# Performance work log

Measured on AMD Instinct MI355X. Metric: run time of the kernel, lower is better.

## Reference

```python
import jax, jax.numpy as jnp
import numpy as np

K = 10
EPS = 1e-5
SLOPE = 0.01
B, FIN, FOUT, N = 16, 128, 128, 2048


def _bn(x, g, b, axes):
    # training-mode batchnorm over given axes (channel dim is axis 1)
    m = jnp.mean(x, axis=axes, keepdims=True)
    v = jnp.var(x, axis=axes, keepdims=True)
    sh = [1] * x.ndim
    sh[1] = -1
    return (x - m) * jax.lax.rsqrt(v + EPS) * g.reshape(sh) + b.reshape(sh)


def _lrelu(x):
    return jnp.where(x >= 0, x, SLOPE * x)


def _conv1x1(x, W, b):
    return jnp.einsum('bcnk,oc->bonk', x, W) + b[None, :, None, None]


def _forward(x, pc, Wf, bf, gf, betaf, Wx, bx, gx, betax, Wa1, ba1, ga1, beta_a1, Wa2, ba2, ga2, beta_a2, Wi, bi, gi, beta_i, W2, b2, g2, beta2):
    Bsz, Fin, Npts = x.shape
    k = K
    # --- kNN graph build: pairwise sq-dist via bmm, full sort, drop self ---
    sq = jnp.sum(x * x, axis=1)  # [B,N]
    dist = -2.0 * jnp.einsum('bdn,bdm->bnm', x, x) + sq[:, :, None] + sq[:, None, :]
    idx = jnp.argsort(dist, axis=2)[:, :, 1:k + 1]  # [B,N,k]
    gather = jax.vmap(lambda f, i: f[:, i])  # [C,N],[N,k] -> [C,N,k]
    nbr = gather(x, idx)
    nbr_xyz = gather(pc, idx)
    e_fea = jnp.concatenate([jnp.broadcast_to(x[..., None], (Bsz, Fin, Npts, k)), nbr - x[..., None]], axis=1)   # [B,2Fin,N,k]
    e_xyz = jnp.concatenate([jnp.broadcast_to(pc[..., None], (Bsz, 3, Npts, k)), nbr_xyz - pc[..., None]], axis=1)  # [B,6,N,k]
    # --- bilateral attention weights ---
    w = _lrelu(_bn(_conv1x1(e_fea, Wf, bf), gf, betaf, (0, 2, 3))) * _lrelu(_bn(_conv1x1(e_xyz, Wx, bx), gx, betax, (0, 2, 3)))
    w = _lrelu(_bn(_conv1x1(w, Wa1, ba1), ga1, beta_a1, (0, 2, 3)))
    w = _lrelu(_bn(_conv1x1(w, Wa2, ba2), ga2, beta_a2, (0, 2, 3)))
    w = jax.nn.softmax(w, axis=-1)  # [B,2Fin,N,k]
    # --- interpolation conv over neighbour axis (kernel [1, k//2+1]) ---
    inte = jax.lax.conv_general_dilated(e_fea, Wi, (1, 1), 'VALID', dimension_numbers=('NCHW', 'OIHW', 'NCHW')) + bi[None, :, None, None]
    inte = _lrelu(_bn(inte, gi, beta_i, (0, 2, 3)))  # [B,4Fin,N,k-k//2]
    inte = jnp.transpose(inte, (0, 2, 1, 3)).reshape(Bsz, Npts, 2 * Fin, k)  # channel-pair interleave, same layout as torch .view
    inte = jnp.transpose(inte, (0, 2, 1, 3)) * w  # [B,2Fin,N,k]
    merge = jnp.concatenate([e_fea, inte], axis=3)  # [B,2Fin,N,2k]
    # conv2: kernel [1,2k] spans full width -> width-1 output, as einsum
    out = jnp.einsum('bcnw,ocw->bon', merge, W2[:, :, 0, :]) + b2[None, :, None]  # [B,2Fout,N]
    out = jnp.maximum(_bn(out, g2, beta2, (0, 2)), 0.0)
    Fout = out.shape[1] // 2
    return out.reshape(Bsz, Fout, 2 * Npts)


def setup_inputs() -> dict:
    ks = jax.random.split(jax.random.key(0), 10)
    s = 0.05
    return {
        'x': jax.random.normal(ks[0], (B, FIN, N), jnp.float32),
        'pc': jax.random.normal(ks[1], (B, 3, N), jnp.float32),
        'Wf': jax.random.normal(ks[2], (16, 2 * FIN), jnp.float32) * s,
        'bf': jnp.zeros((16,), jnp.float32), 'gf': jnp.ones((16,), jnp.float32), 'betaf': jnp.zeros((16,), jnp.float32),
        'Wx': jax.random.normal(ks[3], (16, 6), jnp.float32) * s,
        'bx': jnp.zeros((16,), jnp.float32), 'gx': jnp.ones((16,), jnp.float32), 'betax': jnp.zeros((16,), jnp.float32),
        'Wa1': jax.random.normal(ks[4], (64, 16), jnp.float32) * s,
        'ba1': jnp.zeros((64,), jnp.float32), 'ga1': jnp.ones((64,), jnp.float32), 'beta_a1': jnp.zeros((64,), jnp.float32),
        'Wa2': jax.random.normal(ks[5], (2 * FIN, 64), jnp.float32) * s,
        'ba2': jnp.zeros((2 * FIN,), jnp.float32), 'ga2': jnp.ones((2 * FIN,), jnp.float32), 'beta_a2': jnp.zeros((2 * FIN,), jnp.float32),
        'Wi': jax.random.normal(ks[6], (4 * FIN, 2 * FIN, 1, K // 2 + 1), jnp.float32) * s,
        'bi': jnp.zeros((4 * FIN,), jnp.float32), 'gi': jnp.ones((4 * FIN,), jnp.float32), 'beta_i': jnp.zeros((4 * FIN,), jnp.float32),
        'W2': jax.random.normal(ks[7], (2 * FOUT, 2 * FIN, 1, 2 * K), jnp.float32) * s,
        'b2': jnp.zeros((2 * FOUT,), jnp.float32), 'g2': jnp.ones((2 * FOUT,), jnp.float32), 'beta2': jnp.zeros((2 * FOUT,), jnp.float32),
    }


def reference(x, pc, Wf, bf, gf, betaf, Wx, bx, gx, betax, Wa1, ba1, ga1, beta_a1, Wa2, ba2, ga2, beta_a2, Wi, bi, gi, beta_i, W2, b2, g2, beta2):
    return _forward(x, pc, Wf, bf, gf, betaf, Wx, bx, gx, betax, Wa1, ba1, ga1, beta_a1, Wa2, ba2, ga2, beta_a2, Wi, bi, gi, beta_i, W2, b2, g2, beta2)
```

## Files before the change

kernel.cpp:

```cpp
#include <hip/hip_runtime.h>
#include <hip/hip_bf16.h>
#include <cstdio>
#include <cstddef>

#define B_    16
#define FIN_  128
#define N_    2048
#define K_    10
#define EPS_  1e-5f
#define SLOPE_ 0.01f

typedef float f32x4 __attribute__((ext_vector_type(4)));
typedef short s16x8 __attribute__((ext_vector_type(8)));
typedef short s16x4 __attribute__((ext_vector_type(4)));

constexpr int SUM_F=0,   SS_F=16,   SUM_X=32,  SS_X=48;
constexpr int SUM_A1=64, SS_A1=128, SUM_A2=192,SS_A2=448;
constexpr int SUM_I=704, SS_I=1216, SUM_O=1728,SS_O=1984;
constexpr int SCALE_F=2240, SHIFT_F=2256, SCALE_X=2272, SHIFT_X=2288;
constexpr int SCALE_A1=2304, SHIFT_A1=2368, SCALE_A2=2432, SHIFT_A2=2688;
constexpr int SCALE_I=2944, SHIFT_I=3456, SCALE_O=3968, SHIFT_O=4224;
constexpr int STATS_TOTAL=4480;

constexpr int KW2_ = 3968;
constexpr int CHUNK_ = 8192;

__device__ __forceinline__ float lrelu(float v){ return v >= 0.f ? v : SLOPE_*v; }
__device__ __forceinline__ float wave_sum(float v){
  #pragma unroll
  for (int o = 32; o > 0; o >>= 1) v += __shfl_down(v, o, 64);
  return v;
}
__device__ __forceinline__ unsigned short f2bf(float f){
  __hip_bfloat16 h = __float2bfloat16(f);
  return *reinterpret_cast<unsigned short*>(&h);
}
__device__ __forceinline__ float bf2f(unsigned short u){
  __hip_bfloat16 h = *reinterpret_cast<__hip_bfloat16*>(&u);
  return __bfloat162float(h);
}

__global__ void k_zero(float* s){
  for (int i = threadIdx.x; i < STATS_TOTAL; i += 256) s[i] = 0.f;
}

__global__ __launch_bounds__(256) void k_xt(const float* __restrict__ x, float* __restrict__ xT){
  __shared__ float t[32][33];
  const int b = blockIdx.z;
  const int c0 = blockIdx.x*32, n0 = blockIdx.y*32;
  const int tx = threadIdx.x & 31, ty = threadIdx.x >> 5;
  #pragma unroll
  for (int s = 0; s < 32; s += 8)
    t[ty+s][tx] = x[((size_t)b*FIN_ + c0+ty+s)*N_ + n0 + tx];
  __syncthreads();
  #pragma unroll
  for (int s = 0; s < 32; s += 8)
    xT[((size_t)b*N_ + n0+ty+s)*FIN_ + c0 + tx] = t[tx][ty+s];
}

__global__ __launch_bounds__(256) void k_sq(const float* __restrict__ x, float* __restrict__ sq){
  int id = blockIdx.x*256 + threadIdx.x;
  int b = id >> 11, n = id & (N_-1);
  const float* xb = x + (size_t)b*FIN_*N_ + n;
  float part[16];
  #pragma unroll
  for (int p = 0; p < 16; ++p){
    float a = 0.f;
    #pragma unroll
    for (int q = 0; q < 8; ++q){
      float v = xb[(size_t)(p + 16*q)*N_];
      a = __fmaf_rn(v, v, a);
    }
    part[p] = a;
  }
  #pragma unroll
  for (int off = 8; off > 0; off >>= 1){
    #pragma unroll
    for (int l = 0; l < off; ++l)
      part[l] = __fadd_rn(part[l], part[l+off]);
  }
  sq[id] = part[0];
}

__global__ __launch_bounds__(256, 2) void k_knn(const float* __restrict__ x, const float* __restrict__ sq,
                                                int* __restrict__ idx){
  __shared__ __align__(16) char smem[61440];
  float* xi = (float*)smem;
  const int b = blockIdx.y, i0 = blockIdx.x*64;
  const float* xb = x + (size_t)b*FIN_*N_;
  for (int t = threadIdx.x; t < FIN_*64; t += 256){
    int c = t >> 6, ii = t & 63;
    xi[t] = xb[(size_t)c*N_ + i0 + ii];
  }
  __syncthreads();
  const int ty = threadIdx.x >> 4;
  const int tx = threadIdx.x & 15;
  const int ibase = ty*4;
  const f32x4 sqi = *(const f32x4*)&sq[b*N_ + i0 + ibase];
  float bd[4][10]; int bi[4][10];
  #pragma unroll
  for (int ii=0;ii<4;++ii)
    #pragma unroll
    for (int s=0;s<10;++s){ bd[ii][s]=1e30f; bi[ii][s]=-1; }

  for (int j0 = 0; j0 < N_; j0 += 64){
    const int jb = j0 + tx*4;
    const float* xjp = xb + jb;
    f32x4 acc[4] = {};
    #pragma unroll 8
    for (int c = 0; c < FIN_; ++c){
      const f32x4 a  = *(const f32x4*)&xi[c*64 + ibase];
      const f32x4 bb = *(const f32x4*)&xjp[(size_t)c*N_];
      #pragma unroll
      for (int ii=0;ii<4;++ii){
        #pragma unroll
        for (int m=0;m<4;++m)
          acc[ii][m] = __fmaf_rn(a[ii], bb[m], acc[ii][m]);
      }
    }
    const f32x4 sqj = *(const f32x4*)&sq[b*N_ + jb];
    #pragma unroll
    for (int ii=0;ii<4;++ii){
      const int i = i0 + ibase + ii;
      #pragma unroll
      for (int m=0;m<4;++m){
        int j = jb + m;
        float d = __fadd_rn(__fadd_rn(__fmul_rn(-2.f, acc[ii][m]), sqi[ii]), sqj[m]);
        if (j == i) d = 1e30f;
        if (d < bd[ii][9]){
          bd[ii][9] = d; bi[ii][9] = j;
          #pragma unroll
          for (int s = 9; s > 0; --s){
            if (bd[ii][s] < bd[ii][s-1]){
              float td = bd[ii][s]; bd[ii][s] = bd[ii][s-1]; bd[ii][s-1] = td;
              int ti = bi[ii][s]; bi[ii][s] = bi[ii][s-1]; bi[ii][s-1] = ti;
            }
          }
        }
      }
    }
  }

  __syncthreads();
  float* dbuf = (float*)smem;
  unsigned short* ibuf = (unsigned short*)(smem + 40960);
  #pragma unroll
  for (int ii=0;ii<4;++ii)
    #pragma unroll
    for (int s=0;s<10;++s){
      dbuf[(tx*10+s)*64 + ibase+ii] = bd[ii][s];
      ibuf[(tx*10+s)*64 + ibase+ii] = (unsigned short)bi[ii][s];
    }
  __syncthreads();
  if (threadIdx.x < 64){
    const int rr = threadIdx.x;
    int p[16];
    #pragma unroll
    for (int qq=0;qq<16;++qq) p[qq]=0;
    int* op = idx + ((size_t)b*N_ + i0 + rr)*K_;
    for (int s = 0; s < K_; ++s){
      float dm = 1e38f; int im = 0x7fffffff; int qm = 0;
      #pragma unroll
      for (int qq = 0; qq < 16; ++qq){
        int pq = p[qq];
        float d  = (pq < 10) ? dbuf[(qq*10+pq)*64 + rr] : 1e38f;
        int   jd = (pq < 10) ? (int)ibuf[(qq*10+pq)*64 + rr] : 0x7fffffff;
        bool take = (d < dm) || (d == dm && jd < im);
        if (take){ dm = d; im = jd; qm = qq; }
      }
      #pragma unroll
      for (int qq = 0; qq < 16; ++qq) if (qm == qq) p[qq]++;
      op[s] = im;
    }
  }
}

__global__ __launch_bounds__(256) void k_fx_stats(const float* __restrict__ xT, const float* __restrict__ pc,
                                                  const int* __restrict__ idx,
                                                  const float* __restrict__ Wf, const float* __restrict__ Wx,
                                                  float* __restrict__ stats, float* __restrict__ ytmp){
  __shared__ float wfT[256*16];
  __shared__ float wxT[6*16];
  for (int t = threadIdx.x; t < 256*16; t += 256){ int c = t >> 4, o = t & 15; wfT[t] = Wf[o*256 + c]; }
  if (threadIdx.x < 96){ int cc = threadIdx.x >> 4, o = threadIdx.x & 15; wxT[cc*16+o] = Wx[o*6+cc]; }
  __syncthreads();
  const int id = blockIdx.x*256 + threadIdx.x;
  const int b = id >> 11, n = id & (N_-1);
  const float* xs = xT + (size_t)id*FIN_;
  const float* pb = pc + (size_t)b*3*N_;
  float yc[16];
  #pragma unroll
  for (int o=0;o<16;++o) yc[o]=0.f;
  for (int c=0;c<FIN_;c+=4){
    const f32x4 v4 = *(const f32x4*)&xs[c];
    #pragma unroll
    for (int e=0;e<4;++e){
      float v = v4[e];
      #pragma unroll
      for (int o=0;o<16;++o) yc[o] += wfT[(c+e)*16+o]*v;
    }
  }
  float p0=pb[n], p1=pb[N_+n], p2=pb[2*N_+n];
  float sf[16], ssf[16], sx[16], ssx[16];
  #pragma unroll
  for (int o=0;o<16;++o){ sf[o]=0.f;ssf[o]=0.f;sx[o]=0.f;ssx[o]=0.f; }
  for (int kk=0;kk<K_;++kk){
    int j = idx[(size_t)id*K_ + kk];
    const float* xj = xT + ((size_t)b*N_ + j)*FIN_;
    float y[16];
    #pragma unroll
    for (int o=0;o<16;++o) y[o]=yc[o];
    for (int c=0;c<FIN_;c+=4){
      const f32x4 a4 = *(const f32x4*)&xj[c];
      const f32x4 s4 = *(const f32x4*)&xs[c];
      #pragma unroll
      for (int e=0;e<4;++e){
        float d = a4[e]-s4[e];
        #pragma unroll
        for (int o=0;o<16;++o) y[o] += wfT[(128+c+e)*16+o]*d;
      }
    }
    float q0=pb[j]-p0, q1=pb[N_+j]-p1, q2=pb[2*N_+j]-p2;
    float vx[16];
    #pragma unroll
    for (int o=0;o<16;++o){
      vx[o] = wxT[0*16+o]*p0 + wxT[1*16+o]*p1 + wxT[2*16+o]*p2
            + wxT[3*16+o]*q0 + wxT[4*16+o]*q1 + wxT[5*16+o]*q2;
    }
    #pragma unroll
    for (int o=0;o<16;++o){
      sf[o]+=y[o]; ssf[o]+=y[o]*y[o];
      sx[o]+=vx[o]; ssx[o]+=vx[o]*vx[o];
    }
    float* yt = ytmp + ((size_t)id*K_ + kk)*32;
    #pragma unroll
    for (int o=0;o<16;++o){ yt[o] = y[o]; yt[16+o] = vx[o]; }
  }
  #pragma unroll
  for (int o=0;o<16;++o){
    float v;
    v = wave_sum(sf[o]);  if ((threadIdx.x&63)==0) atomicAdd(&stats[SUM_F+o], v);
    v = wave_sum(ssf[o]); if ((threadIdx.x&63)==0) atomicAdd(&stats[SS_F+o], v);
    v = wave_sum(sx[o]);  if ((threadIdx.x&63)==0) atomicAdd(&stats[SUM_X+o], v);
    v = wave_sum(ssx[o]); if ((threadIdx.x&63)==0) atomicAdd(&stats[SS_X+o], v);
  }
}

__global__ void k_finalize(float* stats, int sumoff, int ssoff, int nch, float cnt_inv,
                           const float* __restrict__ g, const float* __restrict__ bt,
                           int scoff, int shoff){
  int c = threadIdx.x;
  if (c < nch){
    float mean = stats[sumoff+c]*cnt_inv;
    float var  = stats[ssoff+c]*cnt_inv - mean*mean;
    float rstd = rsqrtf(var + EPS_);
    float sc = g[c]*rstd;
    stats[scoff+c] = sc;
    stats[shoff+c] = bt[c] - mean*sc;
  }
}

__global__ __launch_bounds__(256) void k_wapply(const float* __restrict__ ytmp, const float* __restrict__ stats,
                                                float* __restrict__ wprod){
  __shared__ float s4[64];
  if (threadIdx.x < 64) s4[threadIdx.x] = stats[SCALE_F + threadIdx.x];
  __syncthreads();
  const int e = blockIdx.x*256 + threadIdx.x;
  const float* yt = ytmp + (size_t)e*32;
  float* wp = wprod + (size_t)e*16;
  #pragma unroll
  for (int o=0;o<16;++o){
    float a  = lrelu(yt[o]*s4[o] + s4[16+o]);
    float bb = lrelu(yt[16+o]*s4[32+o] + s4[48+o]);
    wp[o] = a*bb;
  }
}

__global__ __launch_bounds__(256) void k_a1_stats(const float* __restrict__ wprod, const float* __restrict__ Wa1,
                                                  float* __restrict__ stats){
  __shared__ float wp[64*16];
  const int oc = threadIdx.x & 63, sub = threadIdx.x >> 6;
  float wa[16];
  #pragma unroll
  for (int j = 0; j < 16; ++j) wa[j] = Wa1[oc*16+j];
  float s = 0.f, ss = 0.f;
  for (int tile = blockIdx.x; tile < 5120; tile += gridDim.x){
    __syncthreads();
    for (int t = threadIdx.x; t < 1024; t += 256) wp[t] = wprod[(size_t)tile*1024 + t];
    __syncthreads();
    for (int p = sub*16; p < sub*16+16; ++p){
      float y = 0.f;
      #pragma unroll
      for (int j = 0; j < 16; ++j) y += wa[j]*wp[p*16+j];
      s += y; ss += y*y;
    }
  }
  atomicAdd(&stats[SUM_A1+oc], s);
  atomicAdd(&stats[SS_A1+oc], ss);
}

__global__ __launch_bounds__(256) void k_a2_stats(const float* __restrict__ wprod, const float* __restrict__ Wa1,
                                                  const float* __restrict__ Wa2, float* __restrict__ stats){
  __shared__ float wp[64*16];
  __shared__ float a1t[64*64];
  __shared__ float wa1T[16*64];
  __shared__ float sc1[64], sh1[64];
  for (int t=threadIdx.x;t<1024;t+=256){ int j=t&63, jj=t>>6; wa1T[jj*64+j] = Wa1[j*16+jj]; }
  if (threadIdx.x < 64){ sc1[threadIdx.x]=stats[SCALE_A1+threadIdx.x]; sh1[threadIdx.x]=stats[SHIFT_A1+threadIdx.x]; }
  const int oc = threadIdx.x;
  float wa2[64];
  #pragma unroll
  for (int j=0;j<64;++j) wa2[j] = Wa2[oc*64+j];
  float s=0.f, ss=0.f;
  for (int tile = blockIdx.x; tile < 5120; tile += gridDim.x){
    __syncthreads();
    for (int t=threadIdx.x;t<1024;t+=256) wp[t] = wprod[(size_t)tile*1024 + t];
    __syncthreads();
    for (int t=threadIdx.x;t<4096;t+=256){
      int p = t >> 6, j = t & 63;
      float yv=0.f;
      #pragma unroll
      for (int jj=0;jj<16;++jj) yv += wa1T[jj*64+j]*wp[p*16+jj];
      a1t[t] = lrelu(yv*sc1[j]+sh1[j]);
    }
    __syncthreads();
    #pragma unroll 4
    for (int p=0;p<64;++p){
      float yv=0.f;
      #pragma unroll
      for (int j=0;j<64;++j) yv += wa2[j]*a1t[p*64+j];
      s += yv; ss += yv*yv;
    }
  }
  atomicAdd(&stats[SUM_A2+oc], s);
  atomicAdd(&stats[SS_A2+oc], ss);
}

__global__ __launch_bounds__(256) void k_prepAi(const float* __restrict__ Wi, unsigned short* __restrict__ Ai){
  const int total = 512*896;
  for (int e = blockIdx.x*256 + threadIdx.x; e < total; e += gridDim.x*256){
    int o = e / 896, k = e - o*896;
    float v;
    if (k < 768){
      int u = k >> 7, c = k & 127;
      v = Wi[(size_t)o*1536 + (128+c)*6 + u];
    } else {
      const float* p = &Wi[(size_t)o*1536 + (size_t)(k-768)*6];
      v = p[0]+p[1]+p[2]+p[3]+p[4]+p[5];
    }
    Ai[e] = f2bf(v);
  }
}

__global__ __launch_bounds__(256) void k_prepA2(const float* __restrict__ W2,
                                                unsigned short* __restrict__ A2hi,
                                                unsigned short* __restrict__ A2lo){
  const int total = 256*KW2_;
  for (int e = blockIdx.x*256 + threadIdx.x; e < total; e += gridDim.x*256){
    int oc = e / KW2_, k = e - oc*KW2_;
    const float* wr = &W2[(size_t)oc*5120];
    float v;
    if (k < 2560){
      int o = k & 511, t5 = k >> 9;
      int cch = o >> 1, w = (o & 1)*5 + t5;
      v = wr[cch*20 + 10 + w];
    } else if (k < 3840){
      int kk = k - 2560; int w = kk >> 7, c = kk & 127;
      v = wr[(128+c)*20 + w];
    } else {
      int c = k - 3840;
      float s = 0.f;
      #pragma unroll
      for (int w = 0; w < 10; ++w) s += wr[c*20+w] - wr[(128+c)*20+w];
      v = s;
    }
    unsigned short hi = f2bf(v);
    float lo = v - bf2f(hi);
    A2hi[e] = hi;
    A2lo[e] = f2bf(lo);
  }
}

__global__ __launch_bounds__(256) void k_gather(const float* __restrict__ xT, const int* __restrict__ idx,
                                                unsigned short* __restrict__ Bd, int pxbase){
  const int e = blockIdx.x*256 + threadIdx.x;
  const int pxl = e >> 4, sub = e & 15;
  const int px = pxbase + pxl;
  const int c0 = sub*8;
  const float* xs = xT + (size_t)px*FIN_ + c0;
  const f32x4 s0 = *(const f32x4*)&xs[0];
  const f32x4 s1 = *(const f32x4*)&xs[4];
  unsigned short* bo = Bd + (size_t)pxl*1408;
  const size_t bb = (size_t)(px >> 11)*N_*FIN_;
  const int* ip = idx + (size_t)px*K_;
  #pragma unroll
  for (int w = 0; w < 10; ++w){
    int j = ip[w];
    const float* xj = xT + bb + (size_t)j*FIN_ + c0;
    const f32x4 a0 = *(const f32x4*)&xj[0];
    const f32x4 a1 = *(const f32x4*)&xj[4];
    unsigned short tw[8];
    tw[0]=f2bf(a0.x-s0.x); tw[1]=f2bf(a0.y-s0.y); tw[2]=f2bf(a0.z-s0.z); tw[3]=f2bf(a0.w-s0.w);
    tw[4]=f2bf(a1.x-s1.x); tw[5]=f2bf(a1.y-s1.y); tw[6]=f2bf(a1.z-s1.z); tw[7]=f2bf(a1.w-s1.w);
    *(s16x8*)&bo[w*128 + c0] = *(const s16x8*)tw;
  }
  unsigned short tw[8];
  tw[0]=f2bf(s0.x); tw[1]=f2bf(s0.y); tw[2]=f2bf(s0.z); tw[3]=f2bf(s0.w);
  tw[4]=f2bf(s1.x); tw[5]=f2bf(s1.y); tw[6]=f2bf(s1.z); tw[7]=f2bf(s1.w);
  *(s16x8*)&bo[1280 + c0] = *(const s16x8*)tw;
}

__global__ __launch_bounds__(256) void k_gemmI(const unsigned short* __restrict__ Bd,
                                               const unsigned short* __restrict__ Ai,
                                               __hip_bfloat16* __restrict__ ybuf, float* __restrict__ stats,
                                               int pxbase){
  __shared__ __align__(16) unsigned short As[128*72];
  __shared__ __align__(16) unsigned short Bs[128*72];
  const int o0 = blockIdx.x * 128;
  const int c0 = blockIdx.y * 128;
  const int t5 = blockIdx.z;
  const int rowA = threadIdx.x >> 1;
  const int kA   = (threadIdx.x & 1)*32;
  const unsigned short* arow = Ai + (size_t)(o0+rowA)*896 + kA;
  const int colJ = threadIdx.x >> 1;
  const int kB   = (threadIdx.x & 1)*32;
  const unsigned short* brow = Bd + (size_t)(c0 + colJ)*1408;
  const int wave = threadIdx.x >> 6, lane = threadIdx.x & 63;
  const int quad = lane >> 4, l16 = lane & 15;
  const int wm = wave & 1, wn = wave >> 1;

  f32x4 acc[4][4] = {};

  for (int k0 = 0; k0 < 896; k0 += 64){
    __syncthreads();
    {
      unsigned short* dst = &As[rowA*72 + kA];
      *(s16x8*)&dst[0]  = *(const s16x8*)&arow[k0+0];
      *(s16x8*)&dst[8]  = *(const s16x8*)&arow[k0+8];
      *(s16x8*)&dst[16] = *(const s16x8*)&arow[k0+16];
      *(s16x8*)&dst[24] = *(const s16x8*)&arow[k0+24];
    }
    {
      const int kk = k0 + kB;
      const unsigned short* src = brow + ((kk < 768) ? ((t5 + (kk >> 7))*128 + (kk & 127))
                                                     : (1280 + (kk - 768)));
      unsigned short* dst = &Bs[colJ*72 + kB];
      *(s16x8*)&dst[0]  = *(const s16x8*)&src[0];
      *(s16x8*)&dst[8]  = *(const s16x8*)&src[8];
      *(s16x8*)&dst[16] = *(const s16x8*)&src[16];
      *(s16x8*)&dst[24] = *(const s16x8*)&src[24];
    }
    __syncthreads();
    #pragma unroll
    for (int ks = 0; ks < 2; ++ks){
      s16x8 af[4], bfr[4];
      #pragma unroll
      for (int mt = 0; mt < 4; ++mt)
        af[mt] = *(const s16x8*)&As[(wm*64 + mt*16 + l16)*72 + ks*32 + quad*8];
      #pragma unroll
      for (int nt = 0; nt < 4; ++nt)
        bfr[nt] = *(const s16x8*)&Bs[(wn*64 + nt*16 + l16)*72 + ks*32 + quad*8];
      #pragma unroll
      for (int mt = 0; mt < 4; ++mt)
        #pragma unroll
        for (int nt = 0; nt < 4; ++nt)
          acc[mt][nt] = __builtin_amdgcn_mfma_f32_16x16x32_bf16(af[mt], bfr[nt], acc[mt][nt], 0, 0, 0);
    }
  }

  __syncthreads();
  float* red = (float*)As;
  red[threadIdx.x] = 0.f;
  __syncthreads();
  #pragma unroll
  for (int mt = 0; mt < 4; ++mt){
    const int rowLbase = wm*64 + mt*16 + quad*4;
    #pragma unroll
    for (int reg = 0; reg < 4; ++reg){
      float s = 0.f, ss = 0.f;
      #pragma unroll
      for (int nt = 0; nt < 4; ++nt){ float v = acc[mt][nt][reg]; s += v; ss += v*v; }
      atomicAdd(&red[(rowLbase+reg)*2+0], s);
      atomicAdd(&red[(rowLbase+reg)*2+1], ss);
    }
  }
  #pragma unroll
  for (int mt = 0; mt < 4; ++mt){
    #pragma unroll
    for (int nt = 0; nt < 4; ++nt){
      const int px = pxbase + c0 + wn*64 + nt*16 + l16;
      const int ob = wm*64 + mt*16 + quad*4;
      s16x4 w;
      #pragma unroll
      for (int reg = 0; reg < 4; ++reg) w[reg] = (short)f2bf(acc[mt][nt][reg]);
      *(s16x4*)&ybuf[(size_t)px*2560 + t5*512 + o0 + ob] = w;
    }
  }
  __syncthreads();
  if (threadIdx.x < 128){
    atomicAdd(&stats[SUM_I + o0 + threadIdx.x], red[threadIdx.x*2+0]);
    atomicAdd(&stats[SS_I + o0 + threadIdx.x], red[threadIdx.x*2+1]);
  }
}

__global__ __launch_bounds__(256, 4) void k_wchain(const float* __restrict__ wprod, const float* __restrict__ Wa1,
                                                   const float* __restrict__ Wa2, const float* __restrict__ stats,
                                                   __hip_bfloat16* __restrict__ ybuf, int pxPerBlk){
  __shared__ float wp[160];
  __shared__ float a1l[640];
  __shared__ float wa1T[16*64];
  __shared__ float sc1[64], sh1[64];
  for (int t = threadIdx.x; t < 1024; t += 256){ int j = t & 63, jj = t >> 6; wa1T[jj*64+j] = Wa1[j*16+jj]; }
  if (threadIdx.x < 64){ sc1[threadIdx.x]=stats[SCALE_A1+threadIdx.x]; sh1[threadIdx.x]=stats[SHIFT_A1+threadIdx.x]; }
  const int c = threadIdx.x;
  f32x4 wa2v[16];
  #pragma unroll
  for (int j4=0;j4<16;++j4) wa2v[j4] = *(const f32x4*)&Wa2[c*64 + j4*4];
  const float sc2 = stats[SCALE_A2+c], sh2 = stats[SHIFT_A2+c];
  const float sci0 = stats[SCALE_I + 2*c], shi0 = stats[SHIFT_I + 2*c];
  const float sci1 = stats[SCALE_I + 2*c+1], shi1 = stats[SHIFT_I + 2*c+1];

  for (int pp = 0; pp < pxPerBlk; ++pp){
    const size_t px = (size_t)blockIdx.x*pxPerBlk + pp;
    __syncthreads();
    if (threadIdx.x < 160) wp[threadIdx.x] = wprod[px*160 + threadIdx.x];
    __syncthreads();
    for (int t = threadIdx.x; t < 640; t += 256){
      int kk = t >> 6, j = t & 63;
      float y=0.f;
      #pragma unroll
      for (int jj=0;jj<16;++jj) y += wa1T[jj*64+j]*wp[kk*16+jj];
      a1l[kk*64+j] = lrelu(y*sc1[j]+sh1[j]);
    }
    __syncthreads();
    float wt[10];
    #pragma unroll
    for (int kk=0;kk<10;++kk){
      f32x4 acc = {0.f,0.f,0.f,0.f};
      #pragma unroll
      for (int j4=0;j4<16;++j4){
        const f32x4 a = *(const f32x4*)&a1l[kk*64 + j4*4];
        acc += wa2v[j4]*a;
      }
      float y = (acc.x+acc.y)+(acc.z+acc.w);
      wt[kk] = lrelu(y*sc2+sh2);
    }
    float mx = wt[0];
    #pragma unroll
    for (int kk=1;kk<10;++kk) mx = fmaxf(mx, wt[kk]);
    float sum = 0.f;
    #pragma unroll
    for (int kk=0;kk<10;++kk){ wt[kk] = __expf(wt[kk]-mx); sum += wt[kk]; }
    float inv = 1.f/sum;
    __hip_bfloat16* yb = ybuf + px*2560;
    #pragma unroll
    for (int q = 0; q < 10; ++q){
      const int t5q = (q < 5) ? q : q-5;
      const int ii  = t5q*512 + 2*c + ((q < 5) ? 0 : 1);
      float v = __bfloat162float(yb[ii]);
      float sc = (q < 5) ? sci0 : sci1;
      float sh = (q < 5) ? shi0 : shi1;
      yb[ii] = __float2bfloat16(lrelu(v*sc+sh) * (wt[q]*inv));
    }
  }
}

__global__ __launch_bounds__(256) void k_w2(const float* __restrict__ xT, const int* __restrict__ idx,
                                            const __hip_bfloat16* __restrict__ inte,
                                            const unsigned short* __restrict__ A2hi,
                                            const unsigned short* __restrict__ A2lo,
                                            float* __restrict__ outpre, float* __restrict__ stats){
  __shared__ __align__(16) unsigned short AsH[128*40];
  __shared__ __align__(16) unsigned short AsL[128*40];
  __shared__ __align__(16) unsigned short BsH[128*40];
  __shared__ __align__(16) unsigned short BsL[128*40];
  __shared__ int sIdx[128*10];
  const int r0 = blockIdx.x * 128;
  const int c0 = blockIdx.y * 128;
  for (int t = threadIdx.x; t < 1280; t += 256) sIdx[t] = idx[(size_t)c0*10 + t];
  const int rowA  = threadIdx.x >> 1;
  const int halfA = threadIdx.x & 1;
  const unsigned short* ahrow = A2hi + (size_t)(r0+rowA)*KW2_ + halfA*16;
  const unsigned short* alrow = A2lo + (size_t)(r0+rowA)*KW2_ + halfA*16;
  const int colJ  = threadIdx.x >> 1;
  const int cHalf = (threadIdx.x & 1)*16;
  const int pxJ   = c0 + colJ;
  const size_t selfJ  = (size_t)pxJ*FIN_;
  const size_t bbaseJ = (size_t)(pxJ >> 11)*N_*FIN_;
  const __hip_bfloat16* ibJ = inte + (size_t)pxJ*2560;
  const int wave = threadIdx.x >> 6, lane = threadIdx.x & 63;
  const int quad = lane >> 4, l16 = lane & 15;
  const int wm = wave & 1, wn = wave >> 1;

  f32x4 acc[4][4] = {};

  for (int k0 = 0; k0 < KW2_; k0 += 32){
    __syncthreads();
    {
      *(s16x8*)&AsH[rowA*40 + halfA*16]     = *(const s16x8*)&ahrow[k0];
      *(s16x8*)&AsH[rowA*40 + halfA*16 + 8] = *(const s16x8*)&ahrow[k0+8];
      *(s16x8*)&AsL[rowA*40 + halfA*16]     = *(const s16x8*)&alrow[k0];
      *(s16x8*)&AsL[rowA*40 + halfA*16 + 8] = *(const s16x8*)&alrow[k0+8];
    }
    if (k0 < 2560){
      *(s16x8*)&BsH[colJ*40 + cHalf]     = *(const s16x8*)(ibJ + k0 + cHalf);
      *(s16x8*)&BsH[colJ*40 + cHalf + 8] = *(const s16x8*)(ibJ + k0 + cHalf + 8);
    } else {
      const float* src;
      if (k0 < 3840){
        const int w  = (k0 - 2560) >> 7;
        const int cb = ((k0 - 2560) & 127) + cHalf;
        const int j  = sIdx[colJ*10 + w];
        src = &xT[bbaseJ + (size_t)j*FIN_ + cb];
      } else {
        src = &xT[selfJ + (k0 - 3840) + cHalf];
      }
      unsigned short th[16], tl[16];
      #pragma unroll
      for (int q = 0; q < 4; ++q){
        const f32x4 v = *(const f32x4*)&src[q*4];
        #pragma unroll
        for (int e2 = 0; e2 < 4; ++e2){
          float f = v[e2];
          unsigned short h = f2bf(f);
          float r = f - bf2f(h);
          th[q*4+e2] = h;
          tl[q*4+e2] = f2bf(r);
        }
      }
      *(s16x8*)&BsH[colJ*40 + cHalf]     = *(const s16x8*)&th[0];
      *(s16x8*)&BsH[colJ*40 + cHalf + 8] = *(const s16x8*)&th[8];
      *(s16x8*)&BsL[colJ*40 + cHalf]     = *(const s16x8*)&tl[0];
      *(s16x8*)&BsL[colJ*40 + cHalf + 8] = *(const s16x8*)&tl[8];
    }
    __syncthreads();
    s16x8 ah[4], al[4], bh[4];
    #pragma unroll
    for (int mt = 0; mt < 4; ++mt){
      ah[mt] = *(const s16x8*)&AsH[(wm*64 + mt*16 + l16)*40 + quad*8];
      al[mt] = *(const s16x8*)&AsL[(wm*64 + mt*16 + l16)*40 + quad*8];
    }
    #pragma unroll
    for (int nt = 0; nt < 4; ++nt)
      bh[nt] = *(const s16x8*)&BsH[(wn*64 + nt*16 + l16)*40 + quad*8];
    #pragma unroll
    for (int mt = 0; mt < 4; ++mt)
      #pragma unroll
      for (int nt = 0; nt < 4; ++nt){
        acc[mt][nt] = __builtin_amdgcn_mfma_f32_16x16x32_bf16(ah[mt], bh[nt], acc[mt][nt], 0, 0, 0);
        acc[mt][nt] = __builtin_amdgcn_mfma_f32_16x16x32_bf16(al[mt], bh[nt], acc[mt][nt], 0, 0, 0);
      }
    if (k0 >= 2560){
      s16x8 bl[4];
      #pragma unroll
      for (int nt = 0; nt < 4; ++nt)
        bl[nt] = *(const s16x8*)&BsL[(wn*64 + nt*16 + l16)*40 + quad*8];
      #pragma unroll
      for (int mt = 0; mt < 4; ++mt)
        #pragma unroll
        for (int nt = 0; nt < 4; ++nt)
          acc[mt][nt] = __builtin_amdgcn_mfma_f32_16x16x32_bf16(ah[mt], bl[nt], acc[mt][nt], 0, 0, 0);
    }
  }

  __syncthreads();
  float* red = (float*)AsH;
  red[threadIdx.x] = 0.f;
  __syncthreads();
  #pragma unroll
  for (int mt = 0; mt < 4; ++mt){
    const int rowLbase = wm*64 + mt*16 + quad*4;
    #pragma unroll
    for (int reg = 0; reg < 4; ++reg){
      float s = 0.f, ss = 0.f;
      #pragma unroll
      for (int nt = 0; nt < 4; ++nt){ float v = acc[mt][nt][reg]; s += v; ss += v*v; }
      atomicAdd(&red[(rowLbase+reg)*2+0], s);
      atomicAdd(&red[(rowLbase+reg)*2+1], ss);
    }
  }
  #pragma unroll
  for (int mt = 0; mt < 4; ++mt){
    #pragma unroll
    for (int nt = 0; nt < 4; ++nt){
      const int col = c0 + wn*64 + nt*16 + l16;
      const int rowb = r0 + wm*64 + mt*16 + quad*4;
      #pragma unroll
      for (int reg = 0; reg < 4; ++reg)
        outpre[(size_t)(rowb+reg)*32768 + col] = acc[mt][nt][reg];
    }
  }
  __syncthreads();
  if (threadIdx.x < 128){
    atomicAdd(&stats[SUM_O + r0 + threadIdx.x], red[threadIdx.x*2+0]);
    atomicAdd(&stats[SS_O + r0 + threadIdx.x], red[threadIdx.x*2+1]);
  }
}

__global__ __launch_bounds__(256) void k_final(const float* __restrict__ outpre, const float* __restrict__ stats,
                                               float* __restrict__ out){
  const unsigned total = (unsigned)B_*128u*4096u;
  for (unsigned e = blockIdx.x*256u + threadIdx.x; e < total; e += gridDim.x*256u){
    unsigned b = e >> 19;
    unsigned rem = e & ((1u<<19)-1u);
    unsigned f = rem >> 12;
    unsigned m = rem & 4095u;
    unsigned half = m >> 11;
    unsigned n = m & 2047u;
    unsigned c = f*2u + half;
    float pre = outpre[(size_t)c*32768 + b*2048 + n];
    float v = pre*stats[SCALE_O+c] + stats[SHIFT_O+c];
    out[e] = fmaxf(v, 0.f);
  }
}

extern "C" void kernel_launch(void* const* d_in, const int* in_sizes, int n_in,
                              void* d_out, int out_size, void* d_ws, size_t ws_size,
                              hipStream_t stream) {
  (void)in_sizes; (void)n_in; (void)out_size;
  const float* x    = (const float*)d_in[0];
  const float* pc   = (const float*)d_in[1];
  const float* Wf   = (const float*)d_in[2];
  const float* gf   = (const float*)d_in[4];
  const float* btf  = (const float*)d_in[5];
  const float* Wx   = (const float*)d_in[6];
  const float* gx   = (const float*)d_in[8];
  const float* btx  = (const float*)d_in[9];
  const float* Wa1  = (const float*)d_in[10];
  const float* ga1  = (const float*)d_in[12];
  const float* bta1 = (const float*)d_in[13];
  const float* Wa2  = (const float*)d_in[14];
  const float* ga2  = (const float*)d_in[16];
  const float* bta2 = (const float*)d_in[17];
  const float* Wi   = (const float*)d_in[18];
  const float* gi   = (const float*)d_in[20];
  const float* bti  = (const float*)d_in[21];
  const float* W2   = (const float*)d_in[22];
  const float* g2   = (const float*)d_in[24];
  const float* bt2  = (const float*)d_in[25];
  float* out = (float*)d_out;

  char* ws = (char*)d_ws;
  float*  stats  = (float*)ws;
  int*    idx    = (int*)  (ws + 32768);
  float*  sq     = (float*)(ws + 1343488);
  float*  wprod  = (float*)(ws + 1605632);
  float*  xT     = (float*)(ws + 22577152);
  unsigned short* A2hi = (unsigned short*)(ws + 39354368);
  unsigned short* A2lo = (unsigned short*)(ws + 41385984);
  float*  outpre = (float*)(ws + 44597248);
  unsigned short* Ai = (unsigned short*)(ws + 44597248);
  unsigned short* Bd = (unsigned short*)(ws + 45645824);
  __hip_bfloat16* ybuf = (__hip_bfloat16*)(ws + 78151680);
  float* ytmp = (float*)(ws + 78151680);
  if (ws_size < 245923840ULL) {
    fprintf(stderr, "kernel_launch: ws_size %zu < required 245923840\n", ws_size);
    return;
  }

  k_zero<<<1, 256, 0, stream>>>(stats);
  k_xt<<<dim3(FIN_/32, N_/32, B_), 256, 0, stream>>>(x, xT);
  k_sq<<<(B_*N_)/256, 256, 0, stream>>>(x, sq);
  k_knn<<<dim3(N_/64, B_), 256, 0, stream>>>(x, sq, idx);
  k_prepAi<<<1024, 256, 0, stream>>>(Wi, Ai);
  k_prepA2<<<1024, 256, 0, stream>>>(W2, A2hi, A2lo);

  k_fx_stats<<<(B_*N_)/256, 256, 0, stream>>>(xT, pc, idx, Wf, Wx, stats, ytmp);
  k_finalize<<<1, 512, 0, stream>>>(stats, SUM_F, SS_F, 16, 1.f/327680.f, gf, btf, SCALE_F, SHIFT_F);
  k_finalize<<<1, 512, 0, stream>>>(stats, SUM_X, SS_X, 16, 1.f/327680.f, gx, btx, SCALE_X, SHIFT_X);

  k_wapply<<<1280, 256, 0, stream>>>(ytmp, stats, wprod);
  k_a1_stats<<<512, 256, 0, stream>>>(wprod, Wa1, stats);
  k_finalize<<<1, 512, 0, stream>>>(stats, SUM_A1, SS_A1, 64, 1.f/327680.f, ga1, bta1, SCALE_A1, SHIFT_A1);

  k_a2_stats<<<512, 256, 0, stream>>>(wprod, Wa1, Wa2, stats);
  k_finalize<<<1, 512, 0, stream>>>(stats, SUM_A2, SS_A2, 256, 1.f/327680.f, ga2, bta2, SCALE_A2, SHIFT_A2);

  for (int ch = 0; ch < (B_*N_)/CHUNK_; ++ch){
    k_gather<<<(CHUNK_*16)/256, 256, 0, stream>>>(xT, idx, Bd, ch*CHUNK_);
    k_gemmI<<<dim3(4, CHUNK_/128, 5), 256, 0, stream>>>(Bd, Ai, ybuf, stats, ch*CHUNK_);
  }
  k_finalize<<<1, 512, 0, stream>>>(stats, SUM_I, SS_I, 512, 1.f/163840.f, gi, bti, SCALE_I, SHIFT_I);

  k_wchain<<<2048, 256, 0, stream>>>(wprod, Wa1, Wa2, stats, ybuf, (B_*N_)/2048);
  k_finalize<<<1, 512, 0, stream>>>(stats, SUM_O, SS_O, 256, 1.f/32768.f, g2, bt2, SCALE_O, SHIFT_O);

  k_w2<<<dim3(2, 256), 256, 0, stream>>>(xT, idx, ybuf, A2hi, A2lo, outpre, stats);
  k_finalize<<<1, 512, 0, stream>>>(stats, SUM_O, SS_O, 256, 1.f/32768.f, g2, bt2, SCALE_O, SHIFT_O);

  k_final<<<4096, 256, 0, stream>>>(outpre, stats, out);
}
```

Before: 2.355 ms.

## Split kNN candidate scan into two halves with a separate merge kernel

The kNN kernel now splits the candidate range in two, so each block scans 1024 candidates instead of 2048. This doubles the grid from 512 to 1024 blocks, and shared memory per block drops so occupancy can rise. Each half writes its sorted top-10 distances and indices to global scratch, and a new small kernel merges the two lists per point. A redundant finalize launch before k_w2 is also removed. The cost is extra global traffic, one more launch, and a reuse of the ybuf region as scratch, which is safe only if ybuf is written later.

New measurement: 3.831 ms. 1.63x slower.

```diff
diff --git a/kernel.cpp b/kernel.cpp
--- a/kernel.cpp
+++ b/kernel.cpp
@@ -82,11 +82,11 @@
   sq[id] = part[0];
 }
 
-__global__ __launch_bounds__(256, 2) void k_knn(const float* __restrict__ x, const float* __restrict__ sq,
-                                                int* __restrict__ idx){
-  __shared__ __align__(16) char smem[61440];
+__global__ __launch_bounds__(256, 4) void k_knn(const float* __restrict__ x, const float* __restrict__ sq,
+                                                float* __restrict__ gld, unsigned short* __restrict__ glj){
+  __shared__ __align__(16) char smem[32768];
   float* xi = (float*)smem;
-  const int b = blockIdx.y, i0 = blockIdx.x*64;
+  const int b = blockIdx.z, i0 = blockIdx.x*64, h = blockIdx.y;
   const float* xb = x + (size_t)b*FIN_*N_;
   for (int t = threadIdx.x; t < FIN_*64; t += 256){
     int c = t >> 6, ii = t & 63;
@@ -103,7 +103,7 @@
     #pragma unroll
     for (int s=0;s<10;++s){ bd[ii][s]=1e30f; bi[ii][s]=-1; }
 
-  for (int j0 = 0; j0 < N_; j0 += 64){
+  for (int j0 = h*1024; j0 < h*1024 + 1024; j0 += 64){
     const int jb = j0 + tx*4;
     const float* xjp = xb + jb;
     f32x4 acc[4] = {};
@@ -141,37 +141,55 @@
     }
   }
 
-  __syncthreads();
-  float* dbuf = (float*)smem;
-  unsigned short* ibuf = (unsigned short*)(smem + 40960);
-  #pragma unroll
-  for (int ii=0;ii<4;++ii)
-    #pragma unroll
-    for (int s=0;s<10;++s){
-      dbuf[(tx*10+s)*64 + ibase+ii] = bd[ii][s];
-      ibuf[(tx*10+s)*64 + ibase+ii] = (unsigned short)bi[ii][s];
-    }
-  __syncthreads();
-  if (threadIdx.x < 64){
-    const int rr = threadIdx.x;
-    int p[16];
-    #pragma unroll
-    for (int qq=0;qq<16;++qq) p[qq]=0;
-    int* op = idx + ((size_t)b*N_ + i0 + rr)*K_;
-    for (int s = 0; s < K_; ++s){
-      float dm = 1e38f; int im = 0x7fffffff; int qm = 0;
-      #pragma unroll
-      for (int qq = 0; qq < 16; ++qq){
-        int pq = p[qq];
-        float d  = (pq < 10) ? dbuf[(qq*10+pq)*64 + rr] : 1e38f;
-        int   jd = (pq < 10) ? (int)ibuf[(qq*10+pq)*64 + rr] : 0x7fffffff;
-        bool take = (d < dm) || (d == dm && jd < im);
-        if (take){ dm = d; im = jd; qm = qq; }
+  float* dl = (float*)smem;
+  unsigned short* jl = (unsigned short*)(smem + 11264);
+  for (int ii = 0; ii < 4; ++ii){
+    __syncthreads();
+    #pragma unroll
+    for (int s = 0; s < 10; ++s){
+      dl[(ty*16+tx)*11 + s] = bd[ii][s];
+      jl[(ty*16+tx)*11 + s] = (unsigned short)bi[ii][s];
+    }
+    __syncthreads();
+    if (threadIdx.x < 16){
+      const int iy = threadIdx.x;
+      int p[16];
+      #pragma unroll
+      for (int qq=0;qq<16;++qq) p[qq]=0;
+      const int gi = b*N_ + i0 + iy*4 + ii;
+      float* od = gld + ((size_t)gi*2 + h)*10;
+      unsigned short* oj = glj + ((size_t)gi*2 + h)*10;
+      for (int s = 0; s < K_; ++s){
+        float dm = 1e38f; int im = 0x7fffffff; int qm = 0;
+        #pragma unroll
+        for (int qq = 0; qq < 16; ++qq){
+          int pq = p[qq];
+          float d  = (pq < 10) ? dl[(iy*16+qq)*11 + pq] : 1e38f;
+          int   jd = (pq < 10) ? (int)jl[(iy*16+qq)*11 + pq] : 0x7fffffff;
+          bool take = (d < dm) || (d == dm && jd < im);
+          if (take){ dm = d; im = jd; qm = qq; }
+        }
+        #pragma unroll
+        for (int qq = 0; qq < 16; ++qq) if (qm == qq) p[qq]++;
+        od[s] = dm; oj[s] = (unsigned short)im;
       }
-      #pragma unroll
-      for (int qq = 0; qq < 16; ++qq) if (qm == qq) p[qq]++;
-      op[s] = im;
-    }
+    }
+  }
+}
+
+__global__ __launch_bounds__(256) void k_knn_m2(const float* __restrict__ gld,
+                                                const unsigned short* __restrict__ glj,
+                                                int* __restrict__ idx){
+  const int i = blockIdx.x*256 + threadIdx.x;
+  const float* d2 = gld + (size_t)i*20;
+  const unsigned short* j2 = glj + (size_t)i*20;
+  int p0 = 0, p1 = 0;
+  int* op = idx + (size_t)i*K_;
+  for (int s = 0; s < K_; ++s){
+    float da = d2[p0], db = d2[10+p1];
+    int ja = (int)j2[p0], jb = (int)j2[10+p1];
+    bool ta = (da < db) || (da == db && ja < jb);
+    if (ta){ op[s] = ja; p0++; } else { op[s] = jb; p1++; }
   }
 }
 
@@ -752,6 +770,8 @@
   unsigned short* Ai = (unsigned short*)(ws + 44597248);
   unsigned short* Bd = (unsigned short*)(ws + 45645824);
   __hip_bfloat16* ybuf = (__hip_bfloat16*)(ws + 78151680);
+  float* gld = (float*)(ws + 78151680);
+  unsigned short* glj = (unsigned short*)(ws + 78151680 + 2621440);
   float* ytmp = (float*)(ws + 78151680);
   if (ws_size < 245923840ULL) {
     fprintf(stderr, "kernel_launch: ws_size %zu < required 245923840\n", ws_size);
@@ -761,7 +781,8 @@
   k_zero<<<1, 256, 0, stream>>>(stats);
   k_xt<<<dim3(FIN_/32, N_/32, B_), 256, 0, stream>>>(x, xT);
   k_sq<<<(B_*N_)/256, 256, 0, stream>>>(x, sq);
-  k_knn<<<dim3(N_/64, B_), 256, 0, stream>>>(x, sq, idx);
+  k_knn<<<dim3(N_/64, 2, B_), 256, 0, stream>>>(x, sq, gld, glj);
+  k_knn_m2<<<(B_*N_)/256, 256, 0, stream>>>(gld, glj, idx);
   k_prepAi<<<1024, 256, 0, stream>>>(Wi, Ai);
   k_prepA2<<<1024, 256, 0, stream>>>(W2, A2hi, A2lo);
 
@@ -783,7 +804,6 @@
   k_finalize<<<1, 512, 0, stream>>>(stats, SUM_I, SS_I, 512, 1.f/163840.f, gi, bti, SCALE_I, SHIFT_I);
 
   k_wchain<<<2048, 256, 0, stream>>>(wprod, Wa1, Wa2, stats, ybuf, (B_*N_)/2048);
-  k_finalize<<<1, 512, 0, stream>>>(stats, SUM_O, SS_O, 256, 1.f/32768.f, g2, bt2, SCALE_O, SHIFT_O);
 
   k_w2<<<dim3(2, 256), 256, 0, stream>>>(xT, idx, ybuf, A2hi, A2lo, outpre, stats);
   k_finalize<<<1, 512, 0, stream>>>(stats, SUM_O, SS_O, 256, 1.f/32768.f, g2, bt2, SCALE_O, SHIFT_O);
```
